# Performance work log

Hardware: AMD Instinct MI355X
Metric: run time of the kernel (lower is better)

The kernel has to match this reference:

```python
import jax, jax.numpy as jnp
from jax import lax
import numpy as np

# --- d12 group tables (dihedral group of order 12 acting on the hex grid) ---
# 7 hexagonal taps embedded in a 3x3 grid: center + 6-ring in cyclic (60 deg) order.
_HEX_POS = [(1, 1), (0, 0), (0, 1), (1, 2), (2, 2), (2, 1), (1, 0)]
_HEX_FLAT = np.array([y * 3 + x for (y, x) in _HEX_POS], dtype=np.int32)  # slots in flattened 3x3


def _compose(a, b):
    # group elements (f, r): i -> (-1)^f * i + r (mod 6). a o b.
    f1, r1 = a
    f2, r2 = b
    return (f1 ^ f2, (r1 + (r2 if f1 == 0 else -r2)) % 6)


def _inv(a):
    f, r = a
    return (0, (-r) % 6) if f == 0 else (1, r)


def _group_tables():
    # perm[g, h] = index of g^{-1} o h  (orientation-channel permutation per output orientation g)
    # tap_src[g, k] = source tap index for target tap k under g^{-1} (kernel rotation/reflection)
    perm = np.zeros((12, 12), dtype=np.int32)
    tap_src = np.zeros((12, 7), dtype=np.int32)
    for g in range(12):
        f, r = divmod(g, 6)
        gi = _inv((f, r))
        for h in range(12):
            fh, rh = divmod(h, 6)
            rf, rr = _compose(gi, (fh, rh))
            perm[g, h] = rf * 6 + rr
        tap_src[g, 0] = 0
        for i in range(6):
            src = (i - r) % 6 if f == 0 else (r - i) % 6
            tap_src[g, 1 + i] = 1 + src
    return perm, tap_src


def _padding_basis(Hp, Wp):
    # (T, I, J): per orientation slot t and padded position (y,x), the source
    # (orientation, row, col). Interior = identity; border pixels are gathered from
    # the opposite chart edge with the orientation's rotation part shifted (+/-1)
    # to stitch icosahedral face boundaries.
    T = np.zeros((12, Hp, Wp), dtype=np.int32)
    I = np.zeros((12, Hp, Wp), dtype=np.int32)
    J = np.zeros((12, Hp, Wp), dtype=np.int32)
    for t in range(12):
        f, r = divmod(t, 6)
        for y in range(Hp):
            for x in range(Wp):
                sy, sx, dt = y, x, 0
                if x == 0:
                    sx, dt = Wp - 2, 1
                elif x == Wp - 1:
                    sx, dt = 1, -1
                if y == 0:
                    sy = Hp - 2
                elif y == Hp - 1:
                    sy = 1
                T[t, y, x] = f * 6 + (r + dt) % 6
                I[t, y, x] = sy
                J[t, y, x] = sx
    return T, I, J


def setup_inputs() -> dict:
    key = jax.random.key(0)
    k1, k2, k3 = jax.random.split(key, 3)
    B, Cin, O, H = 8, 16, 16, 64
    x = jax.random.normal(k1, (B, Cin * 12, H + 2, 5 * H + 2), dtype=jnp.float32)
    weight = jax.random.normal(k2, (O, Cin, 12, 7), dtype=jnp.float32) * 0.05
    bias = jax.random.normal(k3, (O,), dtype=jnp.float32) * 0.05
    return {"x": x, "weight": weight, "bias": bias}


def reference(x, weight, bias):
    O, Cin = weight.shape[0], weight.shape[1]
    B = x.shape[0]
    perm, tap_src = _group_tables()

    # apply_weight_basis: gather-expand (O, Cin, 12, 7) -> (O*12, Cin*12, 3, 3)
    taps = weight[:, :, perm, :]  # (O, Cin, 12g, 12h, 7): orientation-channel permutation
    idx = jnp.broadcast_to(jnp.asarray(tap_src)[None, None, :, None, :], taps.shape[:-1] + (7,))
    taps = jnp.take_along_axis(taps, idx, axis=-1)  # rotated/reflected taps per g
    K9 = jnp.zeros((O, Cin, 12, 12, 9), dtype=weight.dtype)
    K9 = K9.at[..., jnp.asarray(_HEX_FLAT)].set(taps)  # scatter 7 taps into 3x3 (corners stay 0)
    K = K9.reshape(O, Cin, 12, 12, 3, 3).transpose(0, 2, 1, 3, 4, 5).reshape(O * 12, Cin * 12, 3, 3)

    bias_e = jnp.repeat(bias, 12)  # bias[bias_basis]

    out = lax.conv_general_dilated(x, K, (1, 1), "VALID",
                                   dimension_numbers=("NCHW", "OIHW", "NCHW"))
    out = out + bias_e[None, :, None, None]

    # F.pad(out, (1,1,1,1)) then d12.pad: boundary-stitch gather with orientation permutation
    z = jnp.pad(out, ((0, 0), (0, 0), (1, 1), (1, 1)))
    Hp, Wp = z.shape[2], z.shape[3]
    T, I, J = _padding_basis(Hp, Wp)
    zr = z.reshape(B, O, 12, Hp, Wp)
    res = zr[:, :, jnp.asarray(T), jnp.asarray(I), jnp.asarray(J)]  # (B, O, 12, Hp, Wp)
    return res.reshape(B, O * 12, Hp, Wp)
```

## Files before the change

### kernel.cpp

```cpp
#include <hip/hip_runtime.h>

#define NB   8
#define NIC  192
#define NOC  192
#define HP   66
#define WP   322
#define HPWP (HP * WP)

typedef _Float16 f16x8 __attribute__((ext_vector_type(8)));
typedef float    f32x4 __attribute__((ext_vector_type(4)));

__device__ __align__(16) _Float16 g_Ks[6 * 7 * 4 * 192 * 8];
__device__ __align__(16) _Float16 g_xt[NB * 6 * 66 * 4 * 322 * 8];

#define ICCH (66 * 4 * 322 * 8)

__global__ void prep_kernel(const float* __restrict__ w) {
    int tid = blockIdx.x * 256 + threadIdx.x;
    if (tid >= 7 * NOC * NIC) return;
    int ic = tid % NIC;
    int rest = tid / NIC;
    int oc = rest % NOC;
    int t = rest / NOC;
    int o = oc / 12, g = oc % 12;
    int c = ic / 12, h = ic % 12;
    int f = g / 6, r = g % 6;
    int ri = (f == 0) ? (6 - r) % 6 : r;
    int fh = h / 6, rh = h % 6;
    int pf = f ^ fh;
    int pr = (f == 0) ? (ri + rh) % 6 : (ri - rh + 6) % 6;
    int pm = pf * 6 + pr;
    const float* wsrc = w + ((o * 16 + c) * 12 + pm) * 7;
    float v;
    if (t == 0) {
        v = wsrc[0];
    } else {
        int i = t - 1;
        int s = (f == 0) ? (i - r + 6) % 6 : (r - i + 6) % 6;
        v = wsrc[1 + s];
    }
    int icc = ic >> 5, kg = (ic >> 3) & 3, j = ic & 7;
    g_Ks[((((icc * 7) + t) * 4 + kg) * 192 + oc) * 8 + j] = (_Float16)v;
}

__global__ __launch_bounds__(256) void transpose_kernel(const float* __restrict__ x) {
    int id  = blockIdx.x;
    int y   = id % 66;
    int icc = (id / 66) % 6;
    int b   = id / 396;
    int kg   = threadIdx.x >> 6;
    int lane = threadIdx.x & 63;
    const float* src0 = x + ((size_t)b * NIC + icc * 32 + kg * 8) * HPWP + (size_t)y * WP;
    _Float16* dst = g_xt + ((((size_t)(b * 6 + icc) * 66 + y) * 4 + kg) * 322) * 8;
#pragma unroll
    for (int p = 0; p < 6; p++) {
        int col = lane + p * 64;
        if (p < 5 || col < 322) {
            union { f16x8 v8; _Float16 h[8]; } u;
#pragma unroll
            for (int j = 0; j < 8; j++)
                u.h[j] = (_Float16)src0[(size_t)j * HPWP + col];
            *(f16x8*)&dst[col * 8] = u.v8;
        }
    }
}

__device__ __forceinline__ void gload16(const _Float16* g, _Float16* l) {
    __builtin_amdgcn_global_load_lds(
        (const __attribute__((address_space(1))) void*)g,
        (__attribute__((address_space(3))) void*)l, 16, 0, 0);
}

__global__ __launch_bounds__(256, 2) void conv_kernel(
    const float* __restrict__ bias, float* __restrict__ out) {
    __shared__ __align__(16) _Float16 lA[3][6144];
    __shared__ __align__(16) _Float16 lB[2][8960];

    int id = blockIdx.x;
    id = (id & 7) * 160 + (id >> 3);
    int xt5 = id % 5;
    int yt = (id / 5) % 32;
    int b  = id / 160;
    int px0 = xt5 * 64, py0 = yt * 2;

    int tid = threadIdx.x;
    int wave = tid >> 6;
    int lane = tid & 63;
    int kg = lane >> 4, n15 = lane & 15;
    int wm = wave & 1;
    int wn = wave >> 1;

    const _Float16* xtb = g_xt + (size_t)b * (6 * ICCH);

    int gbo[5], lso[5];
#pragma unroll
    for (int k = 0; k < 5; k++) {
        int slot = tid + k * 256;
        if (slot > 1055) slot = 1055;
        int row = slot / 264;
        int rem = slot % 264;
        int kg2 = rem / 66;
        int col = rem % 66;
        gbo[k] = (((py0 + row) * 4 + kg2) * 322 + px0 + col) * 8;
        lso[k] = slot * 8;
    }

    f32x4 acc[6][4] = {};

#define WV3 asm volatile("s_waitcnt vmcnt(3)" ::: "memory")
#define WV8 asm volatile("s_waitcnt vmcnt(8)" ::: "memory")
#define WV0 asm volatile("s_waitcnt vmcnt(0)" ::: "memory")

#define COMPUTE(T, HYv, HXv)                                                   \
    {                                                                          \
        const _Float16* bb = &lB[bi][(((wm + (HYv)) * 4 + kg) * 66 +           \
                                      (HXv) + n15) * 8];                       \
        f16x8 xf[4];                                                           \
        _Pragma("unroll")                                                      \
        for (int ni = 0; ni < 4; ni++)                                         \
            xf[ni] = *(const f16x8*)(bb + ni * (16 * 8));                      \
        __builtin_amdgcn_s_setprio(1);                                         \
        _Pragma("unroll")                                                      \
        for (int mi = 0; mi < 6; mi++) {                                       \
            f16x8 wf = *(const f16x8*)                                         \
                &lA[IA(T)][(kg * 192 + wn * 96 + mi * 16 + n15) * 8];          \
            _Pragma("unroll")                                                  \
            for (int ni = 0; ni < 4; ni++)                                     \
                acc[mi][ni] = __builtin_amdgcn_mfma_f32_16x16x32_f16(          \
                    wf, xf[ni], acc[mi][ni], 0, 0, 0);                         \
        }                                                                      \
        __builtin_amdgcn_s_setprio(0);                                         \
    }

#define STEP(T, WVBLK, HYv, HXv)                                               \
    {                                                                          \
        if ((T) < 6 || icc < 5) {               \
            const _Float16* asrc = kb + ((T) + 1) * 6144;                      \
            gload16(asrc + (tid + 0 * 256) * 8,                                \
                    &lA[JA(T)][(tid + 0 * 256) * 8]);                          \
            gload16(asrc + (tid + 1 * 256) * 8,                                \
                    &lA[JA(T)][(tid + 1 * 256) * 8]);                          \
            gload16(asrc + (tid + 2 * 256) * 8,                                \
                    &lA[JA(T)][(tid + 2 * 256) * 8]);                          \
        }                                                                      \
        WVBLK;                                                                 \
        __builtin_amdgcn_s_barrier();                                          \
        __builtin_amdgcn_sched_barrier(0);                                     \
        if ((T) == 4 && icc < 5) {                   \
            const _Float16* bsrc = xtb + (size_t)(icc + 1) * ICCH;             \
            gload16(bsrc + gbo[0], &lB[bi ^ 1][lso[0]]);                       \
            gload16(bsrc + gbo[1], &lB[bi ^ 1][lso[1]]);                       \
            gload16(bsrc + gbo[2], &lB[bi ^ 1][lso[2]]);                       \
            gload16(bsrc + gbo[3], &lB[bi ^ 1][lso[3]]);                       \
            gload16(bsrc + gbo[4], &lB[bi ^ 1][lso[4]]);                       \
        }                                                                      \
        COMPUTE(T, HYv, HXv);                                                  \
    }

    int ia0 = 0, ia1 = 1, ia2 = 2;
    int bi = 0;
#define IA(T) ((T) == 0 || (T) == 3 || (T) == 6 ? ia0 : ((T) == 1 || (T) == 4 ? ia1 : ia2))
#define JA(T) IA((T) + 1 > 6 ? 0 : (T) + 1)
#undef JA
#define JA(T) ((T) == 2 || (T) == 5 ? ia0 : ((T) == 0 || (T) == 3 || (T) == 6 ? ia1 : ia2))

    {
        const _Float16* bsrc = xtb;
        gload16(bsrc + gbo[0], &lB[0][lso[0]]);
        gload16(bsrc + gbo[1], &lB[0][lso[1]]);
        gload16(bsrc + gbo[2], &lB[0][lso[2]]);
        gload16(bsrc + gbo[3], &lB[0][lso[3]]);
        gload16(bsrc + gbo[4], &lB[0][lso[4]]);
        const _Float16* asrc = g_Ks;
        gload16(asrc + (tid + 0 * 256) * 8, &lA[0][(tid + 0 * 256) * 8]);
        gload16(asrc + (tid + 1 * 256) * 8, &lA[0][(tid + 1 * 256) * 8]);
        gload16(asrc + (tid + 2 * 256) * 8, &lA[0][(tid + 2 * 256) * 8]);
    }

    for (int icc = 0; icc < 6; icc++) {
        const _Float16* kb = g_Ks + icc * (7 * 6144);
        STEP(0, WV3, 1, 1);
        STEP(1, WV3, 0, 0);
        STEP(2, WV3, 0, 1);
        STEP(3, WV3, 1, 2);
        STEP(4, WV3, 2, 2);
        STEP(5, { if (icc < 5) { WV8; } else { WV3; } }, 2, 1);
        STEP(6, { if (icc < 5) { WV3; } else { WV0; } }, 1, 0);
        { int tt = ia0; ia0 = ia1; ia1 = ia2; ia2 = tt; }
        bi ^= 1;
    }
#undef STEP
#undef COMPUTE
#undef IA
#undef JA

    int yo = py0 + 1 + wm;
#pragma unroll
    for (int mi = 0; mi < 6; mi++) {
#pragma unroll
        for (int reg = 0; reg < 4; reg++) {
            int oc = wn * 96 + mi * 16 + kg * 4 + reg;
            float bv = bias[oc / 12];
            size_t base = ((size_t)(b * NOC + oc) * HP + yo) * WP + 1 + px0 + n15;
#pragma unroll
            for (int ni = 0; ni < 4; ni++)
                out[base + ni * 16] = acc[mi][ni][reg] + bv;
        }
    }
}

__global__ void border_kernel(float* __restrict__ out) {
    int tid = blockIdx.x * 256 + threadIdx.x;
    int r  = tid % 772;
    int bc = tid / 772;
    int ch = bc % NOC;
    int b  = bc / NOC;
    int y, xx;
    if (r < 322)      { y = 0;  xx = r; }
    else if (r < 644) { y = 65; xx = r - 322; }
    else if (r < 708) { xx = 0;   y = r - 644 + 1; }
    else              { xx = 321; y = r - 708 + 1; }
    int t = ch % 12;
    int o12 = ch - t;
    int f = t / 6, rr = t % 6;
    int dt = (xx == 0) ? 1 : ((xx == 321) ? -1 : 0);
    int sx = (xx == 0) ? 320 : ((xx == 321) ? 1 : xx);
    int sy = (y == 0) ? 64 : ((y == 65) ? 1 : y);
    int tsrc = f * 6 + (rr + dt + 6) % 6;
    float v = out[((size_t)(b * NOC + o12 + tsrc) * HP + sy) * WP + sx];
    out[((size_t)(b * NOC + ch) * HP + y) * WP + xx] = v;
}

extern "C" void kernel_launch(void* const* d_in, const int* in_sizes, int n_in,
                              void* d_out, int out_size, void* d_ws, size_t ws_size,
                              hipStream_t stream) {
    const float* x    = (const float*)d_in[0];
    const float* w    = (const float*)d_in[1];
    const float* bias = (const float*)d_in[2];
    float* out = (float*)d_out;

    prep_kernel<<<(7 * NOC * NIC + 255) / 256, 256, 0, stream>>>(w);
    transpose_kernel<<<NB * 6 * 66, 256, 0, stream>>>(x);
    conv_kernel<<<1280, 256, 0, stream>>>(bias, out);
    border_kernel<<<(NB * NOC * 772) / 256, 256, 0, stream>>>(out);
}
```

Baseline: 342.3 us.

## Prefetch weight slabs two taps ahead and relayout weights for lane-contiguous LDS reads

Weight slabs are now issued after the barrier and two taps ahead instead of one, using the triple LDS buffer as a deeper pipeline, with two slabs preloaded in the prologue. This is meant to hide more global-to-LDS latency behind the MFMA work. The weight layout is also reordered so each wave reads one contiguous 64-lane chunk per mi, which simplifies addressing and may reduce LDS bank conflicts. The vmcnt wait counts change to match, so a wrong count could create a race or stall.

```diff
diff --git a/kernel.cpp b/kernel.cpp
--- a/kernel.cpp
+++ b/kernel.cpp
@@ -10,10 +10,11 @@
 typedef _Float16 f16x8 __attribute__((ext_vector_type(8)));
 typedef float    f32x4 __attribute__((ext_vector_type(4)));
 
-__device__ __align__(16) _Float16 g_Ks[6 * 7 * 4 * 192 * 8];
+__device__ __align__(16) _Float16 g_Ks[6 * 7 * 12 * 64 * 8];
 __device__ __align__(16) _Float16 g_xt[NB * 6 * 66 * 4 * 322 * 8];
 
-#define ICCH (66 * 4 * 322 * 8)
+#define ICCH  (66 * 4 * 322 * 8)
+#define SLABH (12 * 64 * 8)
 
 __global__ void prep_kernel(const float* __restrict__ w) {
     int tid = blockIdx.x * 256 + threadIdx.x;
@@ -40,7 +41,9 @@
         v = wsrc[1 + s];
     }
     int icc = ic >> 5, kg = (ic >> 3) & 3, j = ic & 7;
-    g_Ks[((((icc * 7) + t) * 4 + kg) * 192 + oc) * 8 + j] = (_Float16)v;
+    int wn2 = oc / 96, mi = (oc % 96) / 16, n15 = oc % 16;
+    g_Ks[((((icc * 7) + t) * 12 + mi * 2 + wn2) * 64 + kg * 16 + n15) * 8 + j]
+        = (_Float16)v;
 }
 
 __global__ __launch_bounds__(256) void transpose_kernel(const float* __restrict__ x) {
@@ -73,7 +76,7 @@
 
 __global__ __launch_bounds__(256, 2) void conv_kernel(
     const float* __restrict__ bias, float* __restrict__ out) {
-    __shared__ __align__(16) _Float16 lA[3][6144];
+    __shared__ __align__(16) _Float16 lA[3][SLABH];
     __shared__ __align__(16) _Float16 lB[2][8960];
 
     int id = blockIdx.x;
@@ -110,6 +113,9 @@
 #define WV3 asm volatile("s_waitcnt vmcnt(3)" ::: "memory")
 #define WV8 asm volatile("s_waitcnt vmcnt(8)" ::: "memory")
 #define WV0 asm volatile("s_waitcnt vmcnt(0)" ::: "memory")
+
+#define ABUF(T) ((T) % 3 == 0 ? ia0 : ((T) % 3 == 1 ? ia1 : ia2))
+#define ASTG(T) (((T)+2) % 3 == 0 ? ia0 : (((T)+2) % 3 == 1 ? ia1 : ia2))
 
 #define COMPUTE(T, HYv, HXv)                                                   \
     {                                                                          \
@@ -123,7 +129,7 @@
         _Pragma("unroll")                                                      \
         for (int mi = 0; mi < 6; mi++) {                                       \
             f16x8 wf = *(const f16x8*)                                         \
-                &lA[IA(T)][(kg * 192 + wn * 96 + mi * 16 + n15) * 8];          \
+                &lA[ABUF(T)][((mi * 2 + wn) * 64 + lane) * 8];                 \
             _Pragma("unroll")                                                  \
             for (int ni = 0; ni < 4; ni++)                                     \
                 acc[mi][ni] = __builtin_amdgcn_mfma_f32_16x16x32_f16(          \
@@ -134,18 +140,18 @@
 
 #define STEP(T, WVBLK, HYv, HXv)                                               \
     {                                                                          \
-        if ((T) < 6 || icc < 5) {               \
-            const _Float16* asrc = kb + ((T) + 1) * 6144;                      \
-            gload16(asrc + (tid + 0 * 256) * 8,                                \
-                    &lA[JA(T)][(tid + 0 * 256) * 8]);                          \
-            gload16(asrc + (tid + 1 * 256) * 8,                                \
-                    &lA[JA(T)][(tid + 1 * 256) * 8]);                          \
-            gload16(asrc + (tid + 2 * 256) * 8,                                \
-                    &lA[JA(T)][(tid + 2 * 256) * 8]);                          \
-        }                                                                      \
         WVBLK;                                                                 \
         __builtin_amdgcn_s_barrier();                                          \
         __builtin_amdgcn_sched_barrier(0);                                     \
+        if ((T) < 5 || icc < 5) {  \
+            const _Float16* asrc = kb + ((T) + 2) * SLABH;                     \
+            gload16(asrc + (tid + 0 * 256) * 8,                                \
+                    &lA[ASTG(T)][(tid + 0 * 256) * 8]);                        \
+            gload16(asrc + (tid + 1 * 256) * 8,                                \
+                    &lA[ASTG(T)][(tid + 1 * 256) * 8]);                        \
+            gload16(asrc + (tid + 2 * 256) * 8,                                \
+                    &lA[ASTG(T)][(tid + 2 * 256) * 8]);                        \
+        }                                                                      \
         if ((T) == 4 && icc < 5) {                   \
             const _Float16* bsrc = xtb + (size_t)(icc + 1) * ICCH;             \
             gload16(bsrc + gbo[0], &lB[bi ^ 1][lso[0]]);                       \
@@ -154,15 +160,12 @@
             gload16(bsrc + gbo[3], &lB[bi ^ 1][lso[3]]);                       \
             gload16(bsrc + gbo[4], &lB[bi ^ 1][lso[4]]);                       \
         }                                                                      \
+        __builtin_amdgcn_sched_barrier(0);                                     \
         COMPUTE(T, HYv, HXv);                                                  \
     }
 
     int ia0 = 0, ia1 = 1, ia2 = 2;
     int bi = 0;
-#define IA(T) ((T) == 0 || (T) == 3 || (T) == 6 ? ia0 : ((T) == 1 || (T) == 4 ? ia1 : ia2))
-#define JA(T) IA((T) + 1 > 6 ? 0 : (T) + 1)
-#undef JA
-#define JA(T) ((T) == 2 || (T) == 5 ? ia0 : ((T) == 0 || (T) == 3 || (T) == 6 ? ia1 : ia2))
 
     {
         const _Float16* bsrc = xtb;
@@ -171,28 +174,30 @@
         gload16(bsrc + gbo[2], &lB[0][lso[2]]);
         gload16(bsrc + gbo[3], &lB[0][lso[3]]);
         gload16(bsrc + gbo[4], &lB[0][lso[4]]);
-        const _Float16* asrc = g_Ks;
-        gload16(asrc + (tid + 0 * 256) * 8, &lA[0][(tid + 0 * 256) * 8]);
-        gload16(asrc + (tid + 1 * 256) * 8, &lA[0][(tid + 1 * 256) * 8]);
-        gload16(asrc + (tid + 2 * 256) * 8, &lA[0][(tid + 2 * 256) * 8]);
+        gload16(g_Ks + (tid + 0 * 256) * 8, &lA[0][(tid + 0 * 256) * 8]);
+        gload16(g_Ks + (tid + 1 * 256) * 8, &lA[0][(tid + 1 * 256) * 8]);
+        gload16(g_Ks + (tid + 2 * 256) * 8, &lA[0][(tid + 2 * 256) * 8]);
+        gload16(g_Ks + SLABH + (tid + 0 * 256) * 8, &lA[1][(tid + 0 * 256) * 8]);
+        gload16(g_Ks + SLABH + (tid + 1 * 256) * 8, &lA[1][(tid + 1 * 256) * 8]);
+        gload16(g_Ks + SLABH + (tid + 2 * 256) * 8, &lA[1][(tid + 2 * 256) * 8]);
     }
 
     for (int icc = 0; icc < 6; icc++) {
-        const _Float16* kb = g_Ks + icc * (7 * 6144);
+        const _Float16* kb = g_Ks + icc * (7 * SLABH);
         STEP(0, WV3, 1, 1);
         STEP(1, WV3, 0, 0);
         STEP(2, WV3, 0, 1);
         STEP(3, WV3, 1, 2);
         STEP(4, WV3, 2, 2);
         STEP(5, { if (icc < 5) { WV8; } else { WV3; } }, 2, 1);
-        STEP(6, { if (icc < 5) { WV3; } else { WV0; } }, 1, 0);
+        STEP(6, { if (icc < 5) { WV8; } else { WV0; } }, 1, 0);
         { int tt = ia0; ia0 = ia1; ia1 = ia2; ia2 = tt; }
         bi ^= 1;
     }
 #undef STEP
 #undef COMPUTE
-#undef IA
-#undef JA
+#undef ABUF
+#undef ASTG
 
     int yo = py0 + 1 + wm;
 #pragma unroll
```

Result: slower. 352.4 us (+2.9%).
